# Performance work log

Measured on AMD Instinct MI355X. Metric: run time of the kernel, lower is better.

Reference implementation:

```python
import jax, jax.numpy as jnp
import numpy as np

N, D = 8192, 1024

def setup_inputs() -> dict:
    key = jax.random.key(0)
    ks = jax.random.split(key, 7)
    s = 1.0 / np.sqrt(D)  # mimic nn.Linear init scale
    return {
        "embeddings": jax.random.normal(ks[0], (N, D), jnp.float32),
        "Wq": jax.random.normal(ks[1], (D, D), jnp.float32) * s,
        "bq": jax.random.normal(ks[2], (D,), jnp.float32) * s,
        "Wk": jax.random.normal(ks[3], (D, D), jnp.float32) * s,
        "bk": jax.random.normal(ks[4], (D,), jnp.float32) * s,
        "Wv": jax.random.normal(ks[5], (D, D), jnp.float32) * s,
        "bv": jax.random.normal(ks[6], (D,), jnp.float32) * s,
    }

def reference(embeddings, Wq, bq, Wk, bk, Wv, bv):
    # nn.Linear: y = x @ W^T + b; weights here are stored as [out, in] equivalent (square), use x @ W.T
    q = embeddings @ Wq.T + bq          # [N, D]
    k = embeddings @ Wk.T + bk          # [N, D]
    v = embeddings @ Wv.T + bv          # [N, D]
    scores = q @ k.T                    # [N, N]  (unscaled, as in source)
    attn = jax.nn.softmax(scores, axis=-1)
    out = attn @ v                      # [N, D]
    return out[:, None, :]              # [N, 1, D] matching torch broadcasted-matmul output
```

## Files before the change

kernel.cpp:

```cpp
#include <hip/hip_runtime.h>
#include <hip/hip_fp16.h>
#include <cstdint>
#include <cstddef>

typedef _Float16 half8 __attribute__((ext_vector_type(8)));
typedef _Float16 half4 __attribute__((ext_vector_type(4)));
typedef float floatx4 __attribute__((ext_vector_type(4)));
typedef float floatx16 __attribute__((ext_vector_type(16)));

#define N_TOK 8192
#define DIM   1024

#define EPI_F32   0
#define EPI_PART  1

#define FENCE_BARRIER() asm volatile("s_barrier" ::: "memory")
#define WAIT_VM4()      asm volatile("s_waitcnt vmcnt(4)" ::: "memory")
#define WAIT_VM0()      asm volatile("s_waitcnt vmcnt(0)" ::: "memory")

__device__ __forceinline__ void async_tile16(const _Float16* gp, _Float16* lp) {
    __builtin_amdgcn_global_load_lds(
        (const __attribute__((address_space(1))) void*)gp,
        (__attribute__((address_space(3))) void*)lp, 16, 0, 0);
}

template<int EPI, bool FOLD, bool REMAP>
__global__ __launch_bounds__(512)
void gemm8(const _Float16* __restrict__ Ahi, const _Float16* __restrict__ Alo,
           const _Float16* __restrict__ B, int lda, int ldb, int ntiles,
           float* __restrict__ C, int ldc)
{
    __shared__ _Float16 smem[65536];

    int bx = blockIdx.x, by = blockIdx.y, bz = blockIdx.z;
    if constexpr (REMAP) {
        const int gx = gridDim.x, gy = gridDim.y;
        const int gxy = gx * gy;
        const int nb = gxy * gridDim.z;
        const int bid = bz * gxy + by * gx + bx;
        const int nid = (bid & 7) * (nb >> 3) + (bid >> 3);
        bx = nid % gx; by = (nid / gx) % gy; bz = nid / gxy;
    }

    const int tid  = threadIdx.x;
    const int lane = tid & 63;
    const int w    = tid >> 6;
    const int wm   = w >> 2;
    const int wn   = w & 3;
    const int l15  = lane & 15;
    const int l4   = lane >> 4;
    const int row0 = by * 256;
    const int col0 = bx * 256;
    const int kbeg_t = FOLD ? 0 : bz * ntiles;

    const int r_s = tid >> 3;
    const int j_s = tid & 7;

    _Float16* A0 = smem;
    _Float16* B0 = smem + 16384;
    _Float16* A1 = smem + 32768;
    _Float16* B1 = smem + 49152;

    const int co0 = ((l4)     ^ (l15 >> 1)) << 3;
    const int co1 = ((4 + l4) ^ (l15 >> 1)) << 3;

    floatx4 acc[8][4];
#pragma unroll
    for (int mi = 0; mi < 8; mi++)
#pragma unroll
        for (int ni = 0; ni < 4; ni++)
#pragma unroll
            for (int e = 0; e < 4; e++) acc[mi][ni][e] = 0.f;

    half8 af[4][2], bf[4][2];

    auto asrc = [&](int kt) -> const _Float16* {
        int ktc = kt > ntiles - 1 ? ntiles - 1 : kt;
        if constexpr (FOLD) {
            const _Float16* base = (ktc < 16) ? Ahi : Alo;
            return base + (size_t)row0 * lda + (ktc & 15) * 64;
        } else {
            return Ahi + (size_t)row0 * lda + (size_t)(kbeg_t + ktc) * 64;
        }
    };
    auto bsrc = [&](int kt) -> const _Float16* {
        int ktc = kt > ntiles - 1 ? ntiles - 1 : kt;
        const int kk = FOLD ? (ktc & 15) : (kbeg_t + ktc);
        return B + (size_t)col0 * ldb + (size_t)kk * 64;
    };

    auto stage = [&](const _Float16* tile, int ld, int half, _Float16* reg) {
#pragma unroll
        for (int p = 0; p < 2; p++) {
            const int r  = half * 128 + p * 64 + r_s;
            const int jg = j_s ^ ((r >> 1) & 7);
            async_tile16(tile + (size_t)r * ld + jg * 8, reg + r * 64 + j_s * 8);
        }
    };

    auto lda4 = [&](const _Float16* Ab, int mbase) {
#pragma unroll
        for (int m2 = 0; m2 < 4; m2++) {
            const int r = (wm * 128 + (mbase + m2) * 16 + l15) * 64;
            af[m2][0] = *(const half8*)&Ab[r + co0];
            af[m2][1] = *(const half8*)&Ab[r + co1];
        }
    };
    auto ldb2 = [&](const _Float16* Bb, int nbase) {
#pragma unroll
        for (int n2 = 0; n2 < 2; n2++) {
            const int r = (wn * 64 + (nbase + n2) * 16 + l15) * 64;
            bf[nbase + n2][0] = *(const half8*)&Bb[r + co0];
            bf[nbase + n2][1] = *(const half8*)&Bb[r + co1];
        }
    };
    auto quad = [&](int qm, int qn) {
        __builtin_amdgcn_s_setprio(1);
#pragma unroll
        for (int kk = 0; kk < 2; kk++)
#pragma unroll
            for (int m2 = 0; m2 < 4; m2++)
#pragma unroll
                for (int n2 = 0; n2 < 2; n2++)
                    acc[qm * 4 + m2][qn * 2 + n2] =
                        __builtin_amdgcn_mfma_f32_16x16x32_f16(
                            af[m2][kk], bf[qn * 2 + n2][kk],
                            acc[qm * 4 + m2][qn * 2 + n2], 0, 0, 0);
        __builtin_amdgcn_s_setprio(0);
    };

    stage(bsrc(0), ldb, 0, B0); stage(bsrc(0), ldb, 1, B0);
    stage(asrc(0), lda, 0, A0); stage(asrc(0), lda, 1, A0);
    stage(bsrc(1), ldb, 0, B1); stage(bsrc(1), ldb, 1, B1);
    WAIT_VM4();
    FENCE_BARRIER();

    const int NIc = ntiles >> 1;
    for (int i = 0; i < NIc; i++) {
        const int t1 = 2 * i + 1, t2 = 2 * i + 2, t3 = 2 * i + 3;
        ldb2(B0, 0); lda4(A0, 0); stage(asrc(t1), lda, 0, A1);
        FENCE_BARRIER(); quad(0, 0); FENCE_BARRIER();
        ldb2(B0, 2); stage(asrc(t1), lda, 1, A1);
        FENCE_BARRIER(); quad(0, 1); FENCE_BARRIER();
        lda4(A0, 4); stage(bsrc(t2), ldb, 0, B0);
        FENCE_BARRIER(); quad(1, 0); FENCE_BARRIER();
        stage(bsrc(t2), ldb, 1, B0);
        FENCE_BARRIER(); quad(1, 1); WAIT_VM4(); FENCE_BARRIER();
        ldb2(B1, 0); lda4(A1, 0); stage(asrc(t2), lda, 0, A0);
        FENCE_BARRIER(); quad(0, 0); FENCE_BARRIER();
        ldb2(B1, 2); stage(asrc(t2), lda, 1, A0);
        FENCE_BARRIER(); quad(0, 1); FENCE_BARRIER();
        lda4(A1, 4); stage(bsrc(t3), ldb, 0, B1);
        FENCE_BARRIER(); quad(1, 0); FENCE_BARRIER();
        stage(bsrc(t3), ldb, 1, B1);
        FENCE_BARRIER(); quad(1, 1); WAIT_VM4(); FENCE_BARRIER();
    }
    WAIT_VM0();

#pragma unroll
    for (int mi = 0; mi < 8; mi++) {
#pragma unroll
        for (int ni = 0; ni < 4; ni++) {
            const int row = row0 + wm * 128 + mi * 16 + l4 * 4;
            const int col = col0 + wn * 64 + ni * 16 + l15;
#pragma unroll
            for (int r2 = 0; r2 < 4; r2++) {
                const float v = acc[mi][ni][r2];
                if constexpr (EPI == EPI_F32) {
                    C[(size_t)(row + r2) * ldc + col] = v;
                } else {
                    C[(size_t)(row + r2) * ldc + (size_t)bz * DIM + col] = v;
                }
            }
        }
    }
}

template<int BM, int BN, int BK>
__global__ __launch_bounds__(256)
void gemm_qkv(const _Float16* __restrict__ Ehi, const _Float16* __restrict__ Elo,
              const _Float16* __restrict__ W,
              _Float16* __restrict__ qhi, _Float16* __restrict__ qlo,
              _Float16* __restrict__ khi, _Float16* __restrict__ vtr,
              const float* __restrict__ bq, const float* __restrict__ bk,
              const float* __restrict__ bv)
{
    constexpr int MI = BM / 64;
    constexpr int NI = BN / 64;
    constexpr int CPR = BK / 8;
    constexpr int SW  = CPR - 1;
    constexpr int RPP = 2048 / BK;
    constexpr int IA  = BM * BK / 2048;
    constexpr int IB  = BN * BK / 2048;
    constexpr int A_ELTS = BM * BK;
    constexpr int B_ELTS = BN * BK;
    __shared__ _Float16 smem[2 * A_ELTS + B_ELTS];
    constexpr int tAhi = 0;
    constexpr int tAlo = A_ELTS;
    constexpr int tB   = 2 * A_ELTS;

    int bx = blockIdx.x, by = blockIdx.y, bz = blockIdx.z;
    {
        const int gx = gridDim.x, gy = gridDim.y;
        const int gxy = gx * gy;
        const int nb = gxy * gridDim.z;
        const int bid = bz * gxy + by * gx + bx;
        const int nid = (bid & 7) * (nb >> 3) + (bid >> 3);
        bx = nid % gx; by = (nid / gx) % gy; bz = nid / gxy;
    }
    const int unit = bz;
    const bool dolo = (unit < 2);

    const int tid  = threadIdx.x;
    const int row0 = by * BM;
    const int col0 = bx * BN;
    const int lane = tid & 63;
    const int w    = tid >> 6;
    const int wm   = w & 1, wn = w >> 1;
    const int l31  = lane & 31, lhi = lane >> 5;

    floatx16 acc[MI][NI];
#pragma unroll
    for (int mi = 0; mi < MI; mi++)
#pragma unroll
        for (int ni = 0; ni < NI; ni++)
#pragma unroll
            for (int e = 0; e < 16; e++) acc[mi][ni][e] = 0.f;

    const int r_s = tid / CPR;
    const int j_s = tid % CPR;
    const size_t brow0 = (size_t)(unit * DIM + col0);

    for (int k0 = 0; k0 < DIM; k0 += BK) {
        __syncthreads();
#pragma unroll
        for (int i = 0; i < IA; i++) {
            const int r = i * RPP + r_s;
            const int jg = j_s ^ ((r >> 1) & SW);
            async_tile16(Ehi + (size_t)(row0 + r) * DIM + k0 + jg * 8,
                         smem + tAhi + (i * 256 + tid) * 8);
            if (dolo)
                async_tile16(Elo + (size_t)(row0 + r) * DIM + k0 + jg * 8,
                             smem + tAlo + (i * 256 + tid) * 8);
        }
#pragma unroll
        for (int i = 0; i < IB; i++) {
            const int r = i * RPP + r_s;
            const int jg = j_s ^ ((r >> 1) & SW);
            async_tile16(W + (brow0 + r) * DIM + k0 + jg * 8,
                         smem + tB + (i * 256 + tid) * 8);
        }
        __syncthreads();

#pragma unroll
        for (int ks = 0; ks < BK / 16; ks++) {
            half8 af[MI], bf[NI], al[MI];
            const int cb = ks * 2 + lhi;
#pragma unroll
            for (int mi = 0; mi < MI; mi++) {
                const int r = wm * (BM / 2) + mi * 32 + l31;
                const int cj = (cb ^ ((r >> 1) & SW)) * 8;
                af[mi] = *(half8*)&smem[tAhi + r * BK + cj];
                if (dolo) al[mi] = *(half8*)&smem[tAlo + r * BK + cj];
            }
#pragma unroll
            for (int ni = 0; ni < NI; ni++) {
                const int r = wn * (BN / 2) + ni * 32 + l31;
                const int cj = (cb ^ ((r >> 1) & SW)) * 8;
                bf[ni] = *(half8*)&smem[tB + r * BK + cj];
            }
#pragma unroll
            for (int mi = 0; mi < MI; mi++)
#pragma unroll
                for (int ni = 0; ni < NI; ni++)
                    acc[mi][ni] = __builtin_amdgcn_mfma_f32_32x32x16_f16(af[mi], bf[ni], acc[mi][ni], 0, 0, 0);
            if (dolo) {
#pragma unroll
                for (int mi = 0; mi < MI; mi++)
#pragma unroll
                    for (int ni = 0; ni < NI; ni++)
                        acc[mi][ni] = __builtin_amdgcn_mfma_f32_32x32x16_f16(al[mi], bf[ni], acc[mi][ni], 0, 0, 0);
            }
        }
    }

    const float* bias = (unit == 0) ? bq : (unit == 1) ? bk : bv;
#pragma unroll
    for (int mi = 0; mi < MI; mi++) {
#pragma unroll
        for (int ni = 0; ni < NI; ni++) {
            const int colg = col0 + wn * (BN / 2) + ni * 32 + l31;
            const float bb = bias[colg];
            const int base = row0 + wm * (BM / 2) + mi * 32 + 4 * lhi;
#pragma unroll
            for (int g = 0; g < 4; g++) {
                const int rowb = base + 8 * g;
                if (unit == 2) {
                    half4 hv;
#pragma unroll
                    for (int r2 = 0; r2 < 4; r2++) hv[r2] = (_Float16)(acc[mi][ni][4 * g + r2] + bb);
                    *(half4*)&vtr[(size_t)colg * N_TOK + rowb] = hv;
                } else {
#pragma unroll
                    for (int r2 = 0; r2 < 4; r2++) {
                        const int rowg = rowb + r2;
                        const float t = acc[mi][ni][4 * g + r2] + bb;
                        const _Float16 hi = (_Float16)t;
                        if (unit == 0) {
                            qhi[(size_t)rowg * DIM + colg] = hi;
                            qlo[(size_t)rowg * DIM + colg] = (_Float16)(t - (float)hi);
                        } else {
                            khi[(size_t)rowg * DIM + colg] = hi;
                        }
                    }
                }
            }
        }
    }
}

__global__ __launch_bounds__(256)
void split_inputs(const float* __restrict__ E,
                  const float* __restrict__ Wq, const float* __restrict__ Wk, const float* __restrict__ Wv,
                  _Float16* __restrict__ Ehi, _Float16* __restrict__ Elo,
                  _Float16* __restrict__ Wqh, _Float16* __restrict__ Wkh, _Float16* __restrict__ Wvh)
{
    const int u = blockIdx.y;
    const size_t idx = ((size_t)blockIdx.x * 256 + threadIdx.x) * 4;
    const size_t MM = (size_t)DIM * DIM;
    const float* src; _Float16* dhi; _Float16* dlo = nullptr;
    if (u < 8)      { src = E + u * MM;  dhi = Ehi + u * MM; dlo = Elo + u * MM; }
    else if (u == 8){ src = Wq; dhi = Wqh; }
    else if (u == 9){ src = Wk; dhi = Wkh; }
    else            { src = Wv; dhi = Wvh; }
    const float4 f = *(const float4*)(src + idx);
    half4 hh;
    hh[0] = (_Float16)f.x; hh[1] = (_Float16)f.y; hh[2] = (_Float16)f.z; hh[3] = (_Float16)f.w;
    *(half4*)(dhi + idx) = hh;
    if (u < 8) {
        half4 hl;
        hl[0] = (_Float16)(f.x - (float)hh[0]); hl[1] = (_Float16)(f.y - (float)hh[1]);
        hl[2] = (_Float16)(f.z - (float)hh[2]); hl[3] = (_Float16)(f.w - (float)hh[3]);
        *(half4*)(dlo + idx) = hl;
    }
}

__global__ __launch_bounds__(256)
void softmax_rows(float* __restrict__ S, float* __restrict__ inv_l)
{
    __shared__ float srow[N_TOK];
    __shared__ float red[4];
    const int tid = threadIdx.x;
    float* row = S + (size_t)blockIdx.x * N_TOK;

    float mx = -3.0e38f;
#pragma unroll
    for (int i = 0; i < 8; i++) {
        const int v = i * 256 + tid;
        const float4 f = ((const float4*)row)[v];
        ((float4*)srow)[v] = f;
        mx = fmaxf(mx, fmaxf(fmaxf(f.x, f.y), fmaxf(f.z, f.w)));
    }
#pragma unroll
    for (int off = 32; off > 0; off >>= 1) mx = fmaxf(mx, __shfl_down(mx, off));
    if ((tid & 63) == 0) red[tid >> 6] = mx;
    __syncthreads();
    mx = fmaxf(fmaxf(red[0], red[1]), fmaxf(red[2], red[3]));
    __syncthreads();

    float sum = 0.f;
    _Float16* prow = (_Float16*)row;
#pragma unroll
    for (int i = 0; i < 8; i++) {
        const int v = i * 256 + tid;
        const float4 f = ((const float4*)srow)[v];
        const float e0 = __expf(f.x - mx), e1 = __expf(f.y - mx);
        const float e2 = __expf(f.z - mx), e3 = __expf(f.w - mx);
        sum += (e0 + e1) + (e2 + e3);
        half4 h; h[0] = (_Float16)e0; h[1] = (_Float16)e1; h[2] = (_Float16)e2; h[3] = (_Float16)e3;
        ((half4*)prow)[v] = h;
    }
#pragma unroll
    for (int off = 32; off > 0; off >>= 1) sum += __shfl_down(sum, off);
    if ((tid & 63) == 0) red[tid >> 6] = sum;
    __syncthreads();
    if (tid == 0) inv_l[blockIdx.x] = 1.f / (red[0] + red[1] + red[2] + red[3]);
}

__global__ __launch_bounds__(256)
void reduce_pv(const float* __restrict__ Sc, const float* __restrict__ invl,
               float* __restrict__ out)
{
    const int r  = blockIdx.x;
    const int c4 = threadIdx.x;
    const float* p = Sc + (size_t)r * N_TOK + N_TOK / 2 + (size_t)c4 * 4;
    float4 s = *(const float4*)p;
#pragma unroll
    for (int z = 1; z < 4; z++) {
        const float4 t = *(const float4*)(p + (size_t)z * DIM);
        s.x += t.x; s.y += t.y; s.z += t.z; s.w += t.w;
    }
    const float iv = invl[r];
    float4 o; o.x = s.x * iv; o.y = s.y * iv; o.z = s.z * iv; o.w = s.w * iv;
    *(float4*)(out + (size_t)r * DIM + (size_t)c4 * 4) = o;
}

extern "C" void kernel_launch(void* const* d_in, const int* in_sizes, int n_in,
                              void* d_out, int out_size, void* d_ws, size_t ws_size,
                              hipStream_t stream)
{
    const float* E  = (const float*)d_in[0];
    const float* Wq = (const float*)d_in[1];
    const float* bq = (const float*)d_in[2];
    const float* Wk = (const float*)d_in[3];
    const float* bk = (const float*)d_in[4];
    const float* Wv = (const float*)d_in[5];
    const float* bv = (const float*)d_in[6];
    float* out = (float*)d_out;

    char* ws = (char*)d_ws;
    const size_t SZ = (size_t)N_TOK * DIM * sizeof(_Float16);
    const size_t WW = (size_t)DIM * DIM * sizeof(_Float16);
    _Float16* q_hi = (_Float16*)(ws);
    _Float16* q_lo = (_Float16*)(ws + SZ);
    _Float16* k_hi = (_Float16*)(ws + 2 * SZ);
    _Float16* vt   = (_Float16*)(ws + 3 * SZ);
    float*    invl = (float*)(ws + 4 * SZ);
    char*     scratch = ws + 4 * SZ + 65536;
    _Float16* Ehi = (_Float16*)(scratch);
    _Float16* Elo = (_Float16*)(scratch + SZ);
    _Float16* Wqh = (_Float16*)(scratch + 2 * SZ);
    _Float16* Wkh = (_Float16*)(scratch + 2 * SZ + WW);
    _Float16* Wvh = (_Float16*)(scratch + 2 * SZ + 2 * WW);
    float*    Sc  = (float*)(scratch);
    const size_t esplit_bytes = 2 * SZ + 3 * WW;
    const size_t base = 4 * SZ + 65536;

    int NC = 256;
    const int cands[6] = {8192, 4096, 2048, 1024, 512, 256};
    for (int i = 0; i < 6; i++) {
        size_t sc = (size_t)cands[i] * N_TOK * 4;
        size_t need = base + (sc > esplit_bytes ? sc : esplit_bytes);
        if (ws_size >= need) { NC = cands[i]; break; }
    }

    const dim3 blk(256, 1, 1);
    const dim3 blk512(512, 1, 1);
    constexpr int KS = 4;

    split_inputs<<<dim3(DIM * DIM / 1024, 11, 1), blk, 0, stream>>>(
        E, Wq, Wk, Wv, Ehi, Elo, Wqh, Wkh, Wvh);

    gemm_qkv<128, 128, 64><<<dim3(DIM / 128, N_TOK / 128, 3), blk, 0, stream>>>(
        Ehi, Elo, Wqh, q_hi, q_lo, k_hi, vt, bq, bk, bv);

    const int nchunks = N_TOK / NC;
    for (int c = 0; c < nchunks; c++) {
        const size_t roff = (size_t)c * NC;
        gemm8<EPI_F32, true, true><<<dim3(N_TOK / 256, NC / 256, 1), blk512, 0, stream>>>(
            q_hi + roff * DIM, q_lo + roff * DIM, k_hi, DIM, DIM, 32, Sc, N_TOK);
        softmax_rows<<<dim3(NC, 1, 1), blk, 0, stream>>>(Sc, invl + roff);
        gemm8<EPI_PART, false, true><<<dim3(DIM / 256, NC / 256, KS), blk512, 0, stream>>>(
            (const _Float16*)Sc, nullptr, vt, 2 * N_TOK, N_TOK, 32, Sc + N_TOK / 2, N_TOK);
        reduce_pv<<<dim3(NC, 1, 1), blk, 0, stream>>>(Sc, invl + roff, out + roff * DIM);
    }
}
```

Measured before the change: 665.0 us.

## Coarsen GEMM pipeline barriers, template leading dims, keep softmax row in registers

```diff
diff --git a/kernel.cpp b/kernel.cpp
--- a/kernel.cpp
+++ b/kernel.cpp
@@ -24,10 +24,10 @@
         (__attribute__((address_space(3))) void*)lp, 16, 0, 0);
 }
 
-template<int EPI, bool FOLD, bool REMAP>
+template<int EPI, bool FOLD, bool REMAP, int LDA, int LDB>
 __global__ __launch_bounds__(512)
 void gemm8(const _Float16* __restrict__ Ahi, const _Float16* __restrict__ Alo,
-           const _Float16* __restrict__ B, int lda, int ldb, int ntiles,
+           const _Float16* __restrict__ B, int ntiles,
            float* __restrict__ C, int ldc)
 {
     __shared__ _Float16 smem[65536];
@@ -78,23 +78,31 @@
         int ktc = kt > ntiles - 1 ? ntiles - 1 : kt;
         if constexpr (FOLD) {
             const _Float16* base = (ktc < 16) ? Ahi : Alo;
-            return base + (size_t)row0 * lda + (ktc & 15) * 64;
+            return base + (size_t)row0 * LDA + (ktc & 15) * 64;
         } else {
-            return Ahi + (size_t)row0 * lda + (size_t)(kbeg_t + ktc) * 64;
+            return Ahi + (size_t)row0 * LDA + (size_t)(kbeg_t + ktc) * 64;
         }
     };
     auto bsrc = [&](int kt) -> const _Float16* {
         int ktc = kt > ntiles - 1 ? ntiles - 1 : kt;
         const int kk = FOLD ? (ktc & 15) : (kbeg_t + ktc);
-        return B + (size_t)col0 * ldb + (size_t)kk * 64;
-    };
-
-    auto stage = [&](const _Float16* tile, int ld, int half, _Float16* reg) {
+        return B + (size_t)col0 * LDB + (size_t)kk * 64;
+    };
+
+    auto stageA = [&](const _Float16* tile, int half, _Float16* reg) {
 #pragma unroll
         for (int p = 0; p < 2; p++) {
             const int r  = half * 128 + p * 64 + r_s;
             const int jg = j_s ^ ((r >> 1) & 7);
-            async_tile16(tile + (size_t)r * ld + jg * 8, reg + r * 64 + j_s * 8);
+            async_tile16(tile + (size_t)r * LDA + jg * 8, reg + r * 64 + j_s * 8);
+        }
+    };
+    auto stageB = [&](const _Float16* tile, int half, _Float16* reg) {
+#pragma unroll
+        for (int p = 0; p < 2; p++) {
+            const int r  = half * 128 + p * 64 + r_s;
+            const int jg = j_s ^ ((r >> 1) & 7);
+            async_tile16(tile + (size_t)r * LDB + jg * 8, reg + r * 64 + j_s * 8);
         }
     };
 
@@ -129,31 +137,31 @@
         __builtin_amdgcn_s_setprio(0);
     };
 
-    stage(bsrc(0), ldb, 0, B0); stage(bsrc(0), ldb, 1, B0);
-    stage(asrc(0), lda, 0, A0); stage(asrc(0), lda, 1, A0);
-    stage(bsrc(1), ldb, 0, B1); stage(bsrc(1), ldb, 1, B1);
+    stageB(bsrc(0), 0, B0); stageB(bsrc(0), 1, B0);
+    stageA(asrc(0), 0, A0); stageA(asrc(0), 1, A0);
+    stageB(bsrc(1), 0, B1); stageB(bsrc(1), 1, B1);
     WAIT_VM4();
     FENCE_BARRIER();
 
     const int NIc = ntiles >> 1;
     for (int i = 0; i < NIc; i++) {
         const int t1 = 2 * i + 1, t2 = 2 * i + 2, t3 = 2 * i + 3;
-        ldb2(B0, 0); lda4(A0, 0); stage(asrc(t1), lda, 0, A1);
-        FENCE_BARRIER(); quad(0, 0); FENCE_BARRIER();
-        ldb2(B0, 2); stage(asrc(t1), lda, 1, A1);
-        FENCE_BARRIER(); quad(0, 1); FENCE_BARRIER();
-        lda4(A0, 4); stage(bsrc(t2), ldb, 0, B0);
-        FENCE_BARRIER(); quad(1, 0); FENCE_BARRIER();
-        stage(bsrc(t2), ldb, 1, B0);
-        FENCE_BARRIER(); quad(1, 1); WAIT_VM4(); FENCE_BARRIER();
-        ldb2(B1, 0); lda4(A1, 0); stage(asrc(t2), lda, 0, A0);
-        FENCE_BARRIER(); quad(0, 0); FENCE_BARRIER();
-        ldb2(B1, 2); stage(asrc(t2), lda, 1, A0);
-        FENCE_BARRIER(); quad(0, 1); FENCE_BARRIER();
-        lda4(A1, 4); stage(bsrc(t3), ldb, 0, B1);
-        FENCE_BARRIER(); quad(1, 0); FENCE_BARRIER();
-        stage(bsrc(t3), ldb, 1, B1);
-        FENCE_BARRIER(); quad(1, 1); WAIT_VM4(); FENCE_BARRIER();
+        stageA(asrc(t1), 0, A1); stageA(asrc(t1), 1, A1);
+        ldb2(B0, 0); ldb2(B0, 2); lda4(A0, 0);
+        quad(0, 0); quad(0, 1);
+        FENCE_BARRIER();
+        stageB(bsrc(t2), 0, B0); stageB(bsrc(t2), 1, B0);
+        lda4(A0, 4);
+        quad(1, 0); quad(1, 1);
+        WAIT_VM4(); FENCE_BARRIER();
+        stageA(asrc(t2), 0, A0); stageA(asrc(t2), 1, A0);
+        ldb2(B1, 0); ldb2(B1, 2); lda4(A1, 0);
+        quad(0, 0); quad(0, 1);
+        FENCE_BARRIER();
+        stageB(bsrc(t3), 0, B1); stageB(bsrc(t3), 1, B1);
+        lda4(A1, 4);
+        quad(1, 0); quad(1, 1);
+        WAIT_VM4(); FENCE_BARRIER();
     }
     WAIT_VM0();
 
@@ -348,19 +356,18 @@
 __global__ __launch_bounds__(256)
 void softmax_rows(float* __restrict__ S, float* __restrict__ inv_l)
 {
-    __shared__ float srow[N_TOK];
     __shared__ float red[4];
     const int tid = threadIdx.x;
     float* row = S + (size_t)blockIdx.x * N_TOK;
 
+    float4 v0, v1, v2, v3, v4, v5, v6, v7;
     float mx = -3.0e38f;
-#pragma unroll
-    for (int i = 0; i < 8; i++) {
-        const int v = i * 256 + tid;
-        const float4 f = ((const float4*)row)[v];
-        ((float4*)srow)[v] = f;
-        mx = fmaxf(mx, fmaxf(fmaxf(f.x, f.y), fmaxf(f.z, f.w)));
-    }
+#define LOADMAX(VV, I) \
+    VV = ((const float4*)row)[(I) * 256 + tid]; \
+    mx = fmaxf(mx, fmaxf(fmaxf(VV.x, VV.y), fmaxf(VV.z, VV.w)));
+    LOADMAX(v0, 0) LOADMAX(v1, 1) LOADMAX(v2, 2) LOADMAX(v3, 3)
+    LOADMAX(v4, 4) LOADMAX(v5, 5) LOADMAX(v6, 6) LOADMAX(v7, 7)
+#undef LOADMAX
 #pragma unroll
     for (int off = 32; off > 0; off >>= 1) mx = fmaxf(mx, __shfl_down(mx, off));
     if ((tid & 63) == 0) red[tid >> 6] = mx;
@@ -370,16 +377,15 @@
 
     float sum = 0.f;
     _Float16* prow = (_Float16*)row;
-#pragma unroll
-    for (int i = 0; i < 8; i++) {
-        const int v = i * 256 + tid;
-        const float4 f = ((const float4*)srow)[v];
-        const float e0 = __expf(f.x - mx), e1 = __expf(f.y - mx);
-        const float e2 = __expf(f.z - mx), e3 = __expf(f.w - mx);
-        sum += (e0 + e1) + (e2 + e3);
-        half4 h; h[0] = (_Float16)e0; h[1] = (_Float16)e1; h[2] = (_Float16)e2; h[3] = (_Float16)e3;
-        ((half4*)prow)[v] = h;
-    }
+#define EXPSTORE(VV, I) { \
+    const float e0 = __expf(VV.x - mx), e1 = __expf(VV.y - mx); \
+    const float e2 = __expf(VV.z - mx), e3 = __expf(VV.w - mx); \
+    sum += (e0 + e1) + (e2 + e3); \
+    half4 h; h[0] = (_Float16)e0; h[1] = (_Float16)e1; h[2] = (_Float16)e2; h[3] = (_Float16)e3; \
+    ((half4*)prow)[(I) * 256 + tid] = h; }
+    EXPSTORE(v0, 0) EXPSTORE(v1, 1) EXPSTORE(v2, 2) EXPSTORE(v3, 3)
+    EXPSTORE(v4, 4) EXPSTORE(v5, 5) EXPSTORE(v6, 6) EXPSTORE(v7, 7)
+#undef EXPSTORE
 #pragma unroll
     for (int off = 32; off > 0; off >>= 1) sum += __shfl_down(sum, off);
     if ((tid & 63) == 0) red[tid >> 6] = sum;
@@ -457,11 +463,11 @@
     const int nchunks = N_TOK / NC;
     for (int c = 0; c < nchunks; c++) {
         const size_t roff = (size_t)c * NC;
-        gemm8<EPI_F32, true, true><<<dim3(N_TOK / 256, NC / 256, 1), blk512, 0, stream>>>(
-            q_hi + roff * DIM, q_lo + roff * DIM, k_hi, DIM, DIM, 32, Sc, N_TOK);
+        gemm8<EPI_F32, true, true, DIM, DIM><<<dim3(N_TOK / 256, NC / 256, 1), blk512, 0, stream>>>(
+            q_hi + roff * DIM, q_lo + roff * DIM, k_hi, 32, Sc, N_TOK);
         softmax_rows<<<dim3(NC, 1, 1), blk, 0, stream>>>(Sc, invl + roff);
-        gemm8<EPI_PART, false, true><<<dim3(DIM / 256, NC / 256, KS), blk512, 0, stream>>>(
-            (const _Float16*)Sc, nullptr, vt, 2 * N_TOK, N_TOK, 32, Sc + N_TOK / 2, N_TOK);
+        gemm8<EPI_PART, false, true, 2 * N_TOK, N_TOK><<<dim3(DIM / 256, NC / 256, KS), blk512, 0, stream>>>(
+            (const _Float16*)Sc, nullptr, vt, 32, Sc + N_TOK / 2, N_TOK);
         reduce_pv<<<dim3(NC, 1, 1), blk, 0, stream>>>(Sc, invl + roff, out + roff * DIM);
     }
 }
```

Measured after the change: 676.2 us. About the same (+1.7%).
